# Performance work log

Hardware: AMD Instinct MI355X
Metric: run time of the kernel (lower is better)

## Reference

```python
import jax, jax.numpy as jnp
import numpy as np

N = 128                      # reduced state dimension (Q_dim[0])
S = N * (N + 1) // 2         # number of triu pairwise products = 8256
BATCH = 16384                # snapshot columns
_rows, _cols = np.triu_indices(N)
ROWS = jnp.asarray(_rows)    # [S] int32 constants
COLS = jnp.asarray(_cols)


def setup_inputs() -> dict:
    key = jax.random.key(0)
    kx, ka, kb = jax.random.split(key, 3)
    x = jax.random.normal(kx, (N, BATCH), dtype=jnp.float32)
    # learned operators (module inits them to zeros; use small random for a meaningful baseline)
    A = jax.random.normal(ka, (N, N), dtype=jnp.float32) * 0.02
    B = jax.random.normal(kb, (N, S), dtype=jnp.float32) * 0.02
    return {"x": x, "A": A, "B": B}


def reference(x, A, B):
    # quadratic feature expansion: x2[k, :] = x[i_k, :] * x[j_k, :] over triu pairs
    x2 = x[ROWS] * x[COLS]                 # [S, BATCH]
    return A @ x + B @ x2                  # [N, BATCH]
```

## Files before the change

### kernel.cpp

```cpp
#include <hip/hip_runtime.h>


constexpr int N_     = 128;
constexpr int S_     = 8256;
constexpr int BATCH_ = 16384;
constexpr int KTOT   = 8384;
constexpr int NKT    = 131;
constexpr int LD     = 136;
constexpr size_t WT_BYTES = (size_t)KTOT * 128 * 2;
constexpr size_t PP_OFF   = WT_BYTES;

typedef __attribute__((ext_vector_type(8))) _Float16 half8;
typedef __attribute__((ext_vector_type(2))) _Float16 half2t;
typedef __attribute__((ext_vector_type(4))) float f32x4;

__device__ __forceinline__ ushort f2h(float f) {
    _Float16 h = (_Float16)f;
    ushort b; __builtin_memcpy(&b, &h, 2); return b;
}
__device__ __forceinline__ float h2f(ushort b) {
    _Float16 h; __builtin_memcpy(&h, &b, 2); return (float)h;
}
__device__ __forceinline__ half2t duph(ushort b) {
    uint w = ((uint)b << 16) | (uint)b;
    half2t d; __builtin_memcpy(&d, &w, 4); return d;
}
__device__ __forceinline__ half8 mul_bc(half8 w, half2t d) {
    union { half8 h; half2t p[4]; } u, r;
    u.h = w;
    #pragma unroll
    for (int q = 0; q < 4; ++q) r.p[q] = u.p[q] * d;
    return r.h;
}

__device__ __forceinline__ int cumN(int i) {
    if (i <= 0) return 0;
    const int n = i - 1, t = n >> 3, r = n & 7;
    return 16 * i - (4 * t * (t + 1) + r * (t + 1));
}
__device__ __forceinline__ int offR(int i) {
    const int a = i >> 3, b = i & 7;
    const int p = b ? (8 * (b - 1) - (((b - 1) * b) >> 1)) : 0;
    return 28 * a + p;
}
__device__ __forceinline__ int triS(int i) { return i * (257 - i) / 2; }

__global__ __launch_bounds__(256) void build_all(
    const float* __restrict__ A, const float* __restrict__ B,
    ushort* __restrict__ pp, ushort* __restrict__ wt,
    float* __restrict__ out)
{
    const int bid = blockIdx.x, t = threadIdx.x;
    if (bid < 524) {
        const int idx = bid * 256 + t;
        const int ko  = idx >> 7;
        const int m   = idx & 127;
        const int kt = ko >> 3, kk = (ko >> 2) & 1, oct = ko & 3;
        const int lane = oct * 16 + (m & 15);
        const int e0 = kt * 8192 + kk * 4096 + (m >> 6) * 2048 +
                       ((m >> 4) & 3) * 512 + lane * 8;
        float v[8];
        if (ko < 16) {
            const int i0 = ko * 8;
            #pragma unroll
            for (int el = 0; el < 8; ++el) v[el] = A[m * 128 + i0 + el];
        } else if (ko < 992) {
            const int o = ko - 16;
            int i = 0;
            #pragma unroll
            for (int st = 64; st >= 1; st >>= 1) {
                const int c = i + st;
                if (c < 128 && cumN(c) <= o) i = c;
            }
            const int jb = ((i + 7) >> 3) + (o - cumN(i));
            const int s0 = triS(i) + jb * 8 - i;
            const float* bp = B + (size_t)m * S_ + s0;
            #pragma unroll
            for (int el = 0; el < 8; ++el) v[el] = bp[el];
        } else {
            const int kb = ko * 8 - 7936;
            #pragma unroll
            for (int el = 0; el < 8; ++el) {
                const int kloc = kb + el;
                int i = 0;
                #pragma unroll
                for (int st = 64; st >= 1; st >>= 1) {
                    const int c = i + st;
                    if (c < 128 && offR(c) <= kloc) i = c;
                }
                v[el] = B[(size_t)m * S_ + triS(i) + (kloc - offR(i))];
            }
        }
        ushort o8[8];
        #pragma unroll
        for (int el = 0; el < 8; ++el) o8[el] = f2h(v[el]);
        __builtin_memcpy(wt + e0, o8, 16);
    } else if (bid < 780) {
        const int zb = bid - 524;
        f32x4* o4 = (f32x4*)out;
        #pragma unroll
        for (int c = 0; c < 4; ++c)
            o4[(size_t)zb * 2048 + c * 512 + t] = (f32x4){0.f, 0.f, 0.f, 0.f};
    } else {
        const int i = t;
        if (i < 128) {
            pp[i] = (ushort)(i | (0xFFu << 8));
            const int jb0 = (i + 7) >> 3;
            int kb = 128 + cumN(i) * 8;
            for (int jb = jb0; jb < 16; ++jb) {
                #pragma unroll
                for (int e = 0; e < 8; ++e)
                    pp[kb + e] = (ushort)(i | ((jb * 8 + e) << 8));
                kb += 8;
            }
            const int h = (8 - (i & 7)) & 7;
            const int rb = 7936 + offR(i);
            for (int e = 0; e < h; ++e)
                pp[rb + e] = (ushort)(i | ((i + e) << 8));
        }
    }
}

__device__ __forceinline__ void load_af(half8 af[8], const ushort* __restrict__ wt,
                                        int kt, int wm, int lane) {
    const ushort* ab = wt + ((size_t)kt << 13) + (wm << 11) + (lane << 3);
    #pragma unroll
    for (int kk = 0; kk < 2; ++kk)
        #pragma unroll
        for (int mt = 0; mt < 4; ++mt)
            af[kk * 4 + mt] = *(const half8*)(ab + (kk << 12) + (mt << 9));
}

__device__ __forceinline__ void step_nice(f32x4 acc[4][2], const half8 af[8],
                                          uint prc, const ushort* __restrict__ xr0,
                                          const ushort* __restrict__ xr1) {
    const uint i0a = prc & 0xFFu, j0a = (prc >> 8) & 0xFFu;
    const uint i0b = (prc >> 16) & 0xFFu, j0b = prc >> 24;
    const ushort xia0 = xr0[i0a], xia1 = xr1[i0a];
    const ushort xib0 = xr0[i0b], xib1 = xr1[i0b];
    const half8 wa0 = *(const half8*)(xr0 + j0a);
    const half8 wa1 = *(const half8*)(xr1 + j0a);
    const half8 wb0 = *(const half8*)(xr0 + j0b);
    const half8 wb1 = *(const half8*)(xr1 + j0b);

    half8 bfr[2][2];
    bfr[0][0] = mul_bc(wa0, duph(xia0));
    bfr[0][1] = mul_bc(wa1, duph(xia1));
    bfr[1][0] = mul_bc(wb0, duph(xib0));
    bfr[1][1] = mul_bc(wb1, duph(xib1));

    #pragma unroll
    for (int kk = 0; kk < 2; ++kk)
        #pragma unroll
        for (int mt = 0; mt < 4; ++mt)
            #pragma unroll
            for (int nt = 0; nt < 2; ++nt)
                acc[mt][nt] = __builtin_amdgcn_mfma_f32_16x16x32_f16(
                    af[kk * 4 + mt], bfr[kk][nt], acc[mt][nt], 0, 0, 0);
}

__global__ __launch_bounds__(512) void gemm_mfma(
    const float*  __restrict__ x,
    const ushort* __restrict__ wt,
    const ushort* __restrict__ pp,
    float* __restrict__ out)
{
    __shared__ ushort xt[128 * LD];
    __shared__ uint   ppc[NKT * 4];

    const int t    = threadIdx.x;
    const int b0   = blockIdx.x * 128;
    const int sp   = blockIdx.y;
    const int kt0  = sp * 33;
    const int kt1  = (sp == 3) ? NKT : kt0 + 33;
    const int lane = t & 63;
    const int w    = t >> 6;
    const int wm   = w >> 2, wn = w & 3;
    const int l16  = lane & 15, quad = lane >> 4;

    {
        const int n = t & 127, g = t >> 7;
        #pragma unroll
        for (int c = 0; c < 4; ++c) {
            const int rb = g * 32 + c * 8;
            uint ow[4];
            #pragma unroll
            for (int p = 0; p < 4; ++p) {
                const ushort u0 = f2h(x[(size_t)(rb + 2 * p) * BATCH_ + b0 + n]);
                const ushort u1 = f2h(x[(size_t)(rb + 2 * p + 1) * BATCH_ + b0 + n]);
                ow[p] = (uint)u0 | ((uint)u1 << 16);
            }
            __builtin_memcpy(&xt[n * LD + rb], ow, 16);
        }
    }
    for (int idx = t; idx < NKT * 4; idx += 512) {
        const int kt = idx >> 2, q = idx & 3;
        const uint w0 = *(const uint*)(pp + kt * 64 + q * 8);
        const uint w1 = *(const uint*)(pp + kt * 64 + 32 + q * 8);
        ppc[idx] = (w0 & 0xFFFFu) | ((w1 & 0xFFFFu) << 16);
    }
    __syncthreads();

    f32x4 acc[4][2];
    #pragma unroll
    for (int mt = 0; mt < 4; ++mt)
        #pragma unroll
        for (int nt = 0; nt < 2; ++nt)
            acc[mt][nt] = (f32x4){0.f, 0.f, 0.f, 0.f};

    const ushort* xr0 = xt + (wn * 32 + l16) * LD;
    const ushort* xr1 = xr0 + 16 * LD;

    if (sp == 0) {
        for (int kt = 0; kt < 2; ++kt) {
            half8 af[8];
            load_af(af, wt, kt, wm, lane);
            half8 bfr[2][2];
            #pragma unroll
            for (int kk = 0; kk < 2; ++kk) {
                const int off = kt * 64 + kk * 32 + quad * 8;
                bfr[kk][0] = *(const half8*)(xr0 + off);
                bfr[kk][1] = *(const half8*)(xr1 + off);
            }
            #pragma unroll
            for (int kk = 0; kk < 2; ++kk)
                #pragma unroll
                for (int mt = 0; mt < 4; ++mt)
                    #pragma unroll
                    for (int nt = 0; nt < 2; ++nt)
                        acc[mt][nt] = __builtin_amdgcn_mfma_f32_16x16x32_f16(
                            af[kk * 4 + mt], bfr[kk][nt], acc[mt][nt], 0, 0, 0);
        }
    }

    {
        const int s_ni = (kt0 > 2) ? kt0 : 2;
        const int e_ni = (kt1 < 124) ? kt1 : 124;
        int kt = s_ni;
        if (kt < e_ni) {
            half8 afA[8], afB[8];
            load_af(afA, wt, kt, wm, lane);
            uint prc = ppc[kt * 4 + quad];
            while (true) {
                {
                    const int ktn = (kt + 1 < e_ni) ? kt + 1 : kt;
                    load_af(afB, wt, ktn, wm, lane);
                    const uint prn = ppc[ktn * 4 + quad];
                    step_nice(acc, afA, prc, xr0, xr1);
                    prc = prn; ++kt;
                }
                if (kt >= e_ni) break;
                {
                    const int ktn = (kt + 1 < e_ni) ? kt + 1 : kt;
                    load_af(afA, wt, ktn, wm, lane);
                    const uint prn = ppc[ktn * 4 + quad];
                    step_nice(acc, afB, prc, xr0, xr1);
                    prc = prn; ++kt;
                }
                if (kt >= e_ni) break;
            }
        }
    }

    if (sp == 3) {
        for (int kt = 124; kt < NKT; ++kt) {
            half8 af[8];
            load_af(af, wt, kt, wm, lane);
            half8 bfr[2][2];
            #pragma unroll
            for (int kk = 0; kk < 2; ++kk) {
                const int k0 = kt * 64 + kk * 32 + quad * 8;
                const uint4 pk = *(const uint4*)(pp + k0);
                const uint pr4[4] = {pk.x, pk.y, pk.z, pk.w};
                #pragma unroll
                for (int nt = 0; nt < 2; ++nt) {
                    const ushort* xr = nt ? xr1 : xr0;
                    float prods[8];
                    #pragma unroll
                    for (int e = 0; e < 8; ++e) {
                        const uint ent = (pr4[e >> 1] >> ((e & 1) * 16)) & 0xFFFFu;
                        prods[e] = h2f(xr[ent & 0xFFu]) * h2f(xr[ent >> 8]);
                    }
                    union { half8 h; uint w[4]; } bb;
                    #pragma unroll
                    for (int p = 0; p < 4; ++p) {
                        const auto pk2 = __builtin_amdgcn_cvt_pkrtz(
                            prods[2 * p], prods[2 * p + 1]);
                        __builtin_memcpy(&bb.w[p], &pk2, 4);
                    }
                    bfr[kk][nt] = bb.h;
                }
            }
            #pragma unroll
            for (int kk = 0; kk < 2; ++kk)
                #pragma unroll
                for (int mt = 0; mt < 4; ++mt)
                    #pragma unroll
                    for (int nt = 0; nt < 2; ++nt)
                        acc[mt][nt] = __builtin_amdgcn_mfma_f32_16x16x32_f16(
                            af[kk * 4 + mt], bfr[kk][nt], acc[mt][nt], 0, 0, 0);
        }
    }

    #pragma unroll
    for (int mt = 0; mt < 4; ++mt) {
        #pragma unroll
        for (int nt = 0; nt < 2; ++nt) {
            const int mbase = wm * 64 + mt * 16 + quad * 4;
            const size_t col = (size_t)b0 + wn * 32 + nt * 16 + l16;
            #pragma unroll
            for (int r = 0; r < 4; ++r)
                unsafeAtomicAdd(&out[(size_t)(mbase + r) * BATCH_ + col],
                                acc[mt][nt][r]);
        }
    }
}

extern "C" void kernel_launch(void* const* d_in, const int* in_sizes, int n_in,
                              void* d_out, int out_size, void* d_ws, size_t ws_size,
                              hipStream_t stream) {
    const float* x = (const float*)d_in[0];
    const float* A = (const float*)d_in[1];
    const float* B = (const float*)d_in[2];
    float* out = (float*)d_out;

    ushort* wt = (ushort*)d_ws;
    ushort* pp = (ushort*)((char*)d_ws + PP_OFF);

    build_all<<<781, 256, 0, stream>>>(A, B, pp, wt, out);
    gemm_mfma<<<dim3(BATCH_ / 128, 4), 512, 0, stream>>>(x, wt, pp, out);
}
```

Before: 123.1 us.

## Double batch tile per block and swizzle LDS x tile instead of padding

Each block now covers 256 batch columns instead of 128, so every wave computes four 16-column subtiles and reuses each loaded weight fragment across twice as many MFMAs. This halves the total weight traffic from global memory. The padded LDS layout is replaced by an XOR swizzle on the row offset to avoid bank conflicts, and the per-block LDS cache of pair indices is dropped in favour of direct global loads. The costs are more accumulator registers (64 floats), a larger LDS footprint (64KB), and half as many blocks, which may lower occupancy and parallelism.

Result: slower. 128.4 us (+4.3%).

```diff
diff --git a/kernel.cpp b/kernel.cpp
--- a/kernel.cpp
+++ b/kernel.cpp
@@ -6,7 +6,6 @@
 constexpr int BATCH_ = 16384;
 constexpr int KTOT   = 8384;
 constexpr int NKT    = 131;
-constexpr int LD     = 136;
 constexpr size_t WT_BYTES = (size_t)KTOT * 128 * 2;
 constexpr size_t PP_OFF   = WT_BYTES;
 
@@ -131,32 +130,32 @@
             af[kk * 4 + mt] = *(const half8*)(ab + (kk << 12) + (mt << 9));
 }
 
-__device__ __forceinline__ void step_nice(f32x4 acc[4][2], const half8 af[8],
-                                          uint prc, const ushort* __restrict__ xr0,
-                                          const ushort* __restrict__ xr1) {
-    const uint i0a = prc & 0xFFu, j0a = (prc >> 8) & 0xFFu;
-    const uint i0b = (prc >> 16) & 0xFFu, j0b = prc >> 24;
-    const ushort xia0 = xr0[i0a], xia1 = xr1[i0a];
-    const ushort xib0 = xr0[i0b], xib1 = xr1[i0b];
-    const half8 wa0 = *(const half8*)(xr0 + j0a);
-    const half8 wa1 = *(const half8*)(xr1 + j0a);
-    const half8 wb0 = *(const half8*)(xr0 + j0b);
-    const half8 wb1 = *(const half8*)(xr1 + j0b);
-
-    half8 bfr[2][2];
-    bfr[0][0] = mul_bc(wa0, duph(xia0));
-    bfr[0][1] = mul_bc(wa1, duph(xia1));
-    bfr[1][0] = mul_bc(wb0, duph(xib0));
-    bfr[1][1] = mul_bc(wb1, duph(xib1));
-
+__device__ __forceinline__ void step_nice(f32x4 acc[4][4], const half8 af[8],
+                                          uint w0, uint w1,
+                                          const ushort* __restrict__ xbase,
+                                          int sw) {
+    const int ia = (int)(w0 & 0xFFu) ^ sw, ja = (int)((w0 >> 8) & 0xFFu) ^ sw;
+    const int ib = (int)(w1 & 0xFFu) ^ sw, jb = (int)((w1 >> 8) & 0xFFu) ^ sw;
+    ushort xi[2][4];
+    half8  wj[2][4];
+    #pragma unroll
+    for (int nt = 0; nt < 4; ++nt) {
+        const ushort* xb = xbase + nt * 2048;
+        xi[0][nt] = xb[ia];
+        xi[1][nt] = xb[ib];
+        wj[0][nt] = *(const half8*)(xb + ja);
+        wj[1][nt] = *(const half8*)(xb + jb);
+    }
     #pragma unroll
     for (int kk = 0; kk < 2; ++kk)
         #pragma unroll
-        for (int mt = 0; mt < 4; ++mt)
-            #pragma unroll
-            for (int nt = 0; nt < 2; ++nt)
+        for (int nt = 0; nt < 4; ++nt) {
+            const half8 bfr = mul_bc(wj[kk][nt], duph(xi[kk][nt]));
+            #pragma unroll
+            for (int mt = 0; mt < 4; ++mt)
                 acc[mt][nt] = __builtin_amdgcn_mfma_f32_16x16x32_f16(
-                    af[kk * 4 + mt], bfr[kk][nt], acc[mt][nt], 0, 0, 0);
+                    af[kk * 4 + mt], bfr, acc[mt][nt], 0, 0, 0);
+        }
 }
 
 __global__ __launch_bounds__(512) void gemm_mfma(
@@ -165,11 +164,10 @@
     const ushort* __restrict__ pp,
     float* __restrict__ out)
 {
-    __shared__ ushort xt[128 * LD];
-    __shared__ uint   ppc[NKT * 4];
+    __shared__ ushort xt[256 * 128];
 
     const int t    = threadIdx.x;
-    const int b0   = blockIdx.x * 128;
+    const int b0   = blockIdx.x * 256;
     const int sp   = blockIdx.y;
     const int kt0  = sp * 33;
     const int kt1  = (sp == 3) ? NKT : kt0 + 33;
@@ -177,12 +175,14 @@
     const int w    = t >> 6;
     const int wm   = w >> 2, wn = w & 3;
     const int l16  = lane & 15, quad = lane >> 4;
+    const int sw   = (l16 & 7) << 3;
 
     {
-        const int n = t & 127, g = t >> 7;
-        #pragma unroll
-        for (int c = 0; c < 4; ++c) {
-            const int rb = g * 32 + c * 8;
+        const int n = t & 255, g = t >> 8;
+        const int swn = (n & 7) << 3;
+        #pragma unroll
+        for (int c = 0; c < 8; ++c) {
+            const int rb = g * 64 + c * 8;
             uint ow[4];
             #pragma unroll
             for (int p = 0; p < 4; ++p) {
@@ -190,46 +190,36 @@
                 const ushort u1 = f2h(x[(size_t)(rb + 2 * p + 1) * BATCH_ + b0 + n]);
                 ow[p] = (uint)u0 | ((uint)u1 << 16);
             }
-            __builtin_memcpy(&xt[n * LD + rb], ow, 16);
-        }
-    }
-    for (int idx = t; idx < NKT * 4; idx += 512) {
-        const int kt = idx >> 2, q = idx & 3;
-        const uint w0 = *(const uint*)(pp + kt * 64 + q * 8);
-        const uint w1 = *(const uint*)(pp + kt * 64 + 32 + q * 8);
-        ppc[idx] = (w0 & 0xFFFFu) | ((w1 & 0xFFFFu) << 16);
+            __builtin_memcpy(&xt[n * 128 + (rb ^ swn)], ow, 16);
+        }
     }
     __syncthreads();
 
-    f32x4 acc[4][2];
+    f32x4 acc[4][4];
     #pragma unroll
     for (int mt = 0; mt < 4; ++mt)
         #pragma unroll
-        for (int nt = 0; nt < 2; ++nt)
+        for (int nt = 0; nt < 4; ++nt)
             acc[mt][nt] = (f32x4){0.f, 0.f, 0.f, 0.f};
 
-    const ushort* xr0 = xt + (wn * 32 + l16) * LD;
-    const ushort* xr1 = xr0 + 16 * LD;
+    const ushort* xbase = xt + (wn * 64 + l16) * 128;
 
     if (sp == 0) {
         for (int kt = 0; kt < 2; ++kt) {
             half8 af[8];
             load_af(af, wt, kt, wm, lane);
-            half8 bfr[2][2];
             #pragma unroll
             for (int kk = 0; kk < 2; ++kk) {
-                const int off = kt * 64 + kk * 32 + quad * 8;
-                bfr[kk][0] = *(const half8*)(xr0 + off);
-                bfr[kk][1] = *(const half8*)(xr1 + off);
-            }
-            #pragma unroll
-            for (int kk = 0; kk < 2; ++kk)
+                const int off = (kt * 64 + kk * 32 + quad * 8) ^ sw;
                 #pragma unroll
-                for (int mt = 0; mt < 4; ++mt)
+                for (int nt = 0; nt < 4; ++nt) {
+                    const half8 bfr = *(const half8*)(xbase + nt * 2048 + off);
                     #pragma unroll
-                    for (int nt = 0; nt < 2; ++nt)
+                    for (int mt = 0; mt < 4; ++mt)
                         acc[mt][nt] = __builtin_amdgcn_mfma_f32_16x16x32_f16(
-                            af[kk * 4 + mt], bfr[kk][nt], acc[mt][nt], 0, 0, 0);
+                            af[kk * 4 + mt], bfr, acc[mt][nt], 0, 0, 0);
+                }
+            }
         }
     }
 
@@ -240,22 +230,25 @@
         if (kt < e_ni) {
             half8 afA[8], afB[8];
             load_af(afA, wt, kt, wm, lane);
-            uint prc = ppc[kt * 4 + quad];
+            uint w0 = *(const uint*)(pp + kt * 64 + quad * 8);
+            uint w1 = *(const uint*)(pp + kt * 64 + 32 + quad * 8);
             while (true) {
                 {
                     const int ktn = (kt + 1 < e_ni) ? kt + 1 : kt;
                     load_af(afB, wt, ktn, wm, lane);
-                    const uint prn = ppc[ktn * 4 + quad];
-                    step_nice(acc, afA, prc, xr0, xr1);
-                    prc = prn; ++kt;
+                    const uint nw0 = *(const uint*)(pp + ktn * 64 + quad * 8);
+                    const uint nw1 = *(const uint*)(pp + ktn * 64 + 32 + quad * 8);
+                    step_nice(acc, afA, w0, w1, xbase, sw);
+                    w0 = nw0; w1 = nw1; ++kt;
                 }
                 if (kt >= e_ni) break;
                 {
                     const int ktn = (kt + 1 < e_ni) ? kt + 1 : kt;
                     load_af(afA, wt, ktn, wm, lane);
-                    const uint prn = ppc[ktn * 4 + quad];
-                    step_nice(acc, afB, prc, xr0, xr1);
-                    prc = prn; ++kt;
+                    const uint nw0 = *(const uint*)(pp + ktn * 64 + quad * 8);
+                    const uint nw1 = *(const uint*)(pp + ktn * 64 + 32 + quad * 8);
+                    step_nice(acc, afB, w0, w1, xbase, sw);
+                    w0 = nw0; w1 = nw1; ++kt;
                 }
                 if (kt >= e_ni) break;
             }
@@ -266,48 +259,44 @@
         for (int kt = 124; kt < NKT; ++kt) {
             half8 af[8];
             load_af(af, wt, kt, wm, lane);
-            half8 bfr[2][2];
             #pragma unroll
             for (int kk = 0; kk < 2; ++kk) {
                 const int k0 = kt * 64 + kk * 32 + quad * 8;
                 const uint4 pk = *(const uint4*)(pp + k0);
                 const uint pr4[4] = {pk.x, pk.y, pk.z, pk.w};
                 #pragma unroll
-                for (int nt = 0; nt < 2; ++nt) {
-                    const ushort* xr = nt ? xr1 : xr0;
+                for (int nt = 0; nt < 4; ++nt) {
+                    const ushort* xb = xbase + nt * 2048;
                     float prods[8];
                     #pragma unroll
                     for (int e = 0; e < 8; ++e) {
                         const uint ent = (pr4[e >> 1] >> ((e & 1) * 16)) & 0xFFFFu;
-                        prods[e] = h2f(xr[ent & 0xFFu]) * h2f(xr[ent >> 8]);
+                        prods[e] = h2f(xb[(int)(ent & 0xFFu) ^ sw]) *
+                                   h2f(xb[(int)(ent >> 8) ^ sw]);
                     }
-                    union { half8 h; uint w[4]; } bb;
+                    union { half8 h; uint wdw[4]; } bb;
                     #pragma unroll
                     for (int p = 0; p < 4; ++p) {
                         const auto pk2 = __builtin_amdgcn_cvt_pkrtz(
                             prods[2 * p], prods[2 * p + 1]);
-                        __builtin_memcpy(&bb.w[p], &pk2, 4);
+                        __builtin_memcpy(&bb.wdw[p], &pk2, 4);
                     }
-                    bfr[kk][nt] = bb.h;
-                }
-            }
-            #pragma unroll
-            for (int kk = 0; kk < 2; ++kk)
-                #pragma unroll
-                for (int mt = 0; mt < 4; ++mt)
+                    const half8 bfr = bb.h;
                     #pragma unroll
-                    for (int nt = 0; nt < 2; ++nt)
+                    for (int mt = 0; mt < 4; ++mt)
                         acc[mt][nt] = __builtin_amdgcn_mfma_f32_16x16x32_f16(
-                            af[kk * 4 + mt], bfr[kk][nt], acc[mt][nt], 0, 0, 0);
+                            af[kk * 4 + mt], bfr, acc[mt][nt], 0, 0, 0);
+                }
+            }
         }
     }
 
     #pragma unroll
     for (int mt = 0; mt < 4; ++mt) {
         #pragma unroll
-        for (int nt = 0; nt < 2; ++nt) {
+        for (int nt = 0; nt < 4; ++nt) {
             const int mbase = wm * 64 + mt * 16 + quad * 4;
-            const size_t col = (size_t)b0 + wn * 32 + nt * 16 + l16;
+            const size_t col = (size_t)b0 + wn * 64 + nt * 16 + l16;
             #pragma unroll
             for (int r = 0; r < 4; ++r)
                 unsafeAtomicAdd(&out[(size_t)(mbase + r) * BATCH_ + col],
@@ -328,5 +317,5 @@
     ushort* pp = (ushort*)((char*)d_ws + PP_OFF);
 
     build_all<<<781, 256, 0, stream>>>(A, B, pp, wt, out);
-    gemm_mfma<<<dim3(BATCH_ / 128, 4), 512, 0, stream>>>(x, wt, pp, out);
-}
+    gemm_mfma<<<dim3(BATCH_ / 256, 4), 512, 0, stream>>>(x, wt, pp, out);
+}
```
